# Kernel tuning notes

Hardware: AMD Instinct MI355X
Metric: run time of the kernel (lower is better)

Reference implementation:

```python
import jax, jax.numpy as jnp
import numpy as np

B, T, D = 512, 1024, 128
H = 256  # hidden_size
OUT = 1


def setup_inputs() -> dict:
    key = jax.random.key(0)
    ks = jax.random.split(key, 7)
    s1 = 1.0 / np.sqrt(D + H)
    s2 = 1.0 / np.sqrt(2 * H)
    so = 1.0 / np.sqrt(H)
    return {
        "x": jax.random.normal(ks[0], (B, T, D), dtype=jnp.float32),
        "W1": jax.random.normal(ks[1], (D + H, 4 * H), dtype=jnp.float32) * s1,
        "b1": jnp.zeros((4 * H,), dtype=jnp.float32),
        "W2": jax.random.normal(ks[2], (2 * H, 4 * H), dtype=jnp.float32) * s2,
        "b2": jnp.zeros((4 * H,), dtype=jnp.float32),
        "Wout": jax.random.normal(ks[3], (H, OUT), dtype=jnp.float32) * so,
        "bout": jnp.zeros((OUT,), dtype=jnp.float32),
    }


def _cell(h, c, inp, W, b, feats):
    # fused gates: Dense(4*features) on concat([inp, h]); order f, i, g, o
    gates = jnp.concatenate([inp, h], axis=-1) @ W + b
    f = jax.nn.sigmoid(gates[..., :feats])
    i = jax.nn.sigmoid(gates[..., feats:2 * feats])
    g = jnp.tanh(gates[..., 2 * feats:3 * feats])
    o = jax.nn.sigmoid(gates[..., 3 * feats:])
    new_c = f * c + i * g
    new_h = o * jnp.tanh(new_c)
    return new_h, new_c


def reference(x, W1, b1, W2, b2, Wout, bout):
    batch = x.shape[0]
    h1 = jnp.zeros((batch, H), dtype=x.dtype)
    c1 = jnp.zeros((batch, H), dtype=x.dtype)
    h2 = jnp.zeros((batch, H), dtype=x.dtype)
    c2 = jnp.zeros((batch, H), dtype=x.dtype)

    def step(carry, xt):
        h1, c1, h2, c2 = carry
        h1, c1 = _cell(h1, c1, xt, W1, b1, H)
        h2, c2 = _cell(h2, c2, h1, W2, b2, H)
        return (h1, c1, h2, c2), None

    xs = jnp.swapaxes(x, 0, 1)  # [T, B, D]
    (h1, c1, h2, c2), _ = jax.lax.scan(step, (h1, c1, h2, c2), xs)
    # dropout deterministic (training=False) -> identity; prediction from last h2
    return h2 @ Wout + bout
```

## Files before the change

### kernel.cpp

```cpp
#include <hip/hip_runtime.h>
#include <math.h>

#define Tlen  1024
#define Din   128
#define Hdim  256

typedef __attribute__((ext_vector_type(8)))  short short8;
typedef __attribute__((ext_vector_type(16))) short short16;
typedef __attribute__((ext_vector_type(4)))  float f32x4;

#define WS_BAR    0
#define WS_H      1024
#define WS_WLO1   2098176
#define WS_WLO2   2884608
#define ZERO_BYTES (1024 + 1048576)

__device__ __forceinline__ unsigned short f2bf(float f) {
    unsigned u = __float_as_uint(f);
    u += 0x7fffu + ((u >> 16) & 1u);
    return (unsigned short)(u >> 16);
}
__device__ __forceinline__ float bf2f(unsigned short s) {
    return __uint_as_float(((unsigned)s) << 16);
}
__device__ __forceinline__ float sigf(float x) { return 1.0f / (1.0f + __expf(-x)); }
__device__ __forceinline__ float tanh_(float x) {
    x = fminf(fmaxf(x, -15.0f), 15.0f);
    float e = __expf(2.0f * x);
    return (e - 1.0f) / (e + 1.0f);
}

__device__ __forceinline__ void afrag(const unsigned* p, short8& ah, short8& al) {
    union { unsigned long long u[4]; short16 v; } t;
    const unsigned long long* q = (const unsigned long long*)p;
    t.u[0] = __hip_atomic_load(q + 0, __ATOMIC_RELAXED, __HIP_MEMORY_SCOPE_AGENT);
    t.u[1] = __hip_atomic_load(q + 1, __ATOMIC_RELAXED, __HIP_MEMORY_SCOPE_AGENT);
    t.u[2] = __hip_atomic_load(q + 2, __ATOMIC_RELAXED, __HIP_MEMORY_SCOPE_AGENT);
    t.u[3] = __hip_atomic_load(q + 3, __ATOMIC_RELAXED, __HIP_MEMORY_SCOPE_AGENT);
    ah = __builtin_shufflevector(t.v, t.v, 0, 2, 4, 6, 8, 10, 12, 14);
    al = __builtin_shufflevector(t.v, t.v, 1, 3, 5, 7, 9, 11, 13, 15);
}

#define MFMA3(g, AH, AL, BH, BL)                                                   \
    acc[g] = __builtin_amdgcn_mfma_f32_16x16x32_bf16(AH, BH, acc[g], 0, 0, 0);     \
    acc[g] = __builtin_amdgcn_mfma_f32_16x16x32_bf16(AL, BH, acc[g], 0, 0, 0);     \
    acc[g] = __builtin_amdgcn_mfma_f32_16x16x32_bf16(AH, BL, acc[g], 0, 0, 0);

__global__ __launch_bounds__(256, 1) void lstm_persist(
    const float* __restrict__ x,
    const float* __restrict__ W1, const float* __restrict__ b1,
    const float* __restrict__ W2, const float* __restrict__ b2,
    const float* __restrict__ Wout, const float* __restrict__ bout,
    float* __restrict__ out, char* __restrict__ wsb)
{
    __shared__ short8 whi[4096];

    const int tid    = threadIdx.x;
    const int pod    = blockIdx.x & 7;
    const int member = blockIdx.x >> 3;
    const bool is_l1 = (member < 16);
    const int hs     = member & 15;
    const int NKS    = is_l1 ? 12 : 16;
    const float* Wraw = is_l1 ? W1 : W2;
    const float* bias = is_l1 ? b1 : b2;

    short8* blo = (short8*)(wsb + (is_l1 ? (WS_WLO1 + (size_t)hs * 49152)
                                         : (WS_WLO2 + (size_t)hs * 65536)));

    for (int t = tid; t < NKS * 256; t += 256) {
        const int lane = t & 63, g = (t >> 6) & 3, ks = t >> 8;
        const int q = lane >> 4, n = lane & 15;
        const int col = g * 256 + hs * 16 + n;
        short8 hv, lv;
#pragma unroll
        for (int j = 0; j < 8; ++j) {
            float v = Wraw[(size_t)(ks * 32 + q * 8 + j) * 1024 + col];
            unsigned short h = f2bf(v);
            hv[j] = (short)h;
            lv[j] = (short)f2bf(v - bf2f(h));
        }
        whi[t] = hv;
        blo[t] = lv;
    }
    __syncthreads();

    const int w = tid >> 6, lane = tid & 63;
    const int q = lane >> 4, n = lane & 15;
    const int rowA = pod * 64 + w * 16 + n;

    float biasg[4];
#pragma unroll
    for (int g = 0; g < 4; ++g) biasg[g] = bias[g * 256 + hs * 16 + n];

    float creg[4] = {0.f, 0.f, 0.f, 0.f};
    unsigned* bar = (unsigned*)(wsb + WS_BAR) + pod * 32;

    auto plane = [&](int par, int layer) -> unsigned* {
        return (unsigned*)(wsb + WS_H + (size_t)(par ^ 1) * 1048576 + (size_t)layer * 524288);
    };

    for (int p = 0; p <= Tlen; ++p) {
        f32x4 acc[4];
        const bool act_l1 = is_l1 && (p < Tlen);
        const bool act_l2 = (!is_l1) && (p >= 1);

        if (act_l1 || act_l2) {
#pragma unroll
            for (int g = 0; g < 4; ++g) {
                acc[g][0] = biasg[g]; acc[g][1] = biasg[g];
                acc[g][2] = biasg[g]; acc[g][3] = biasg[g];
            }
        }

        if (act_l1) {
#pragma unroll
            for (int ks = 0; ks < 4; ++ks) {
                const int kk = ks * 32 + q * 8;
                const float* xp = x + (size_t)rowA * (size_t)(Tlen * Din) + (size_t)p * Din + kk;
                f32x4 v0 = *(const f32x4*)xp;
                f32x4 v1 = *(const f32x4*)(xp + 4);
                float vv[8] = {v0[0], v0[1], v0[2], v0[3], v1[0], v1[1], v1[2], v1[3]};
                short8 ah, al;
#pragma unroll
                for (int j = 0; j < 8; ++j) {
                    unsigned short h = f2bf(vv[j]);
                    ah[j] = (short)h;
                    al[j] = (short)f2bf(vv[j] - bf2f(h));
                }
#pragma unroll
                for (int g = 0; g < 4; ++g) {
                    short8 bh = whi[ks * 256 + g * 64 + lane];
                    short8 bl = blo[ks * 256 + g * 64 + lane];
                    MFMA3(g, ah, al, bh, bl)
                }
            }
        }

        if (tid == 0 && p > 0) {
            const unsigned tgt = 32u * (unsigned)p;
            while (__hip_atomic_load(bar, __ATOMIC_RELAXED, __HIP_MEMORY_SCOPE_AGENT) < tgt) {}
        }
        __syncthreads();

        if (act_l1) {
            const int s = p;
            const unsigned* h1o = plane((s + 1) & 1, 0);
#pragma unroll
            for (int ks = 4; ks < 12; ++ks) {
                const int kk = ks * 32 + q * 8 - Din;
                short8 ah, al;
                afrag(h1o + (size_t)rowA * Hdim + kk, ah, al);
#pragma unroll
                for (int g = 0; g < 4; ++g) {
                    short8 bh = whi[ks * 256 + g * 64 + lane];
                    short8 bl = blo[ks * 256 + g * 64 + lane];
                    MFMA3(g, ah, al, bh, bl)
                }
            }
            unsigned* op = plane(s & 1, 0);
#pragma unroll
            for (int r = 0; r < 4; ++r) {
                float fg = acc[0][r], ig = acc[1][r], gg = acc[2][r], og = acc[3][r];
                float cn = sigf(fg) * creg[r] + sigf(ig) * tanh_(gg);
                creg[r] = cn;
                float hv = sigf(og) * tanh_(cn);
                const int row = pod * 64 + w * 16 + q * 4 + r;
                const int ci  = hs * 16 + n;
                unsigned short hh = f2bf(hv);
                unsigned short ll = f2bf(hv - bf2f(hh));
                unsigned word = (unsigned)hh | ((unsigned)ll << 16);
                __hip_atomic_store(op + (size_t)row * Hdim + ci, word,
                                   __ATOMIC_RELAXED, __HIP_MEMORY_SCOPE_AGENT);
            }
        }

        if (act_l2) {
            const int s = p - 1;
            const unsigned* h1c = plane(s & 1, 0);
            const unsigned* h2o = plane((s + 1) & 1, 1);
#pragma unroll
            for (int ks = 0; ks < 8; ++ks) {
                const int kk = ks * 32 + q * 8;
                short8 ah, al;
                afrag(h1c + (size_t)rowA * Hdim + kk, ah, al);
#pragma unroll
                for (int g = 0; g < 4; ++g) {
                    short8 bh = whi[ks * 256 + g * 64 + lane];
                    short8 bl = blo[ks * 256 + g * 64 + lane];
                    MFMA3(g, ah, al, bh, bl)
                }
            }
#pragma unroll
            for (int ks = 8; ks < 16; ++ks) {
                const int kk = ks * 32 + q * 8 - 256;
                short8 ah, al;
                afrag(h2o + (size_t)rowA * Hdim + kk, ah, al);
#pragma unroll
                for (int g = 0; g < 4; ++g) {
                    short8 bh = whi[ks * 256 + g * 64 + lane];
                    short8 bl = blo[ks * 256 + g * 64 + lane];
                    MFMA3(g, ah, al, bh, bl)
                }
            }
            unsigned* op = plane(s & 1, 1);
#pragma unroll
            for (int r = 0; r < 4; ++r) {
                float fg = acc[0][r], ig = acc[1][r], gg = acc[2][r], og = acc[3][r];
                float cn = sigf(fg) * creg[r] + sigf(ig) * tanh_(gg);
                creg[r] = cn;
                float hv = sigf(og) * tanh_(cn);
                const int row = pod * 64 + w * 16 + q * 4 + r;
                const int ci  = hs * 16 + n;
                unsigned short hh = f2bf(hv);
                unsigned short ll = f2bf(hv - bf2f(hh));
                unsigned word = (unsigned)hh | ((unsigned)ll << 16);
                __hip_atomic_store(op + (size_t)row * Hdim + ci, word,
                                   __ATOMIC_RELAXED, __HIP_MEMORY_SCOPE_AGENT);
            }
        }

        __syncthreads();
        if (tid == 0) {
            __hip_atomic_fetch_add(bar, 1u, __ATOMIC_RELAXED, __HIP_MEMORY_SCOPE_AGENT);
        }
    }

    if (member == 0) {
        if (tid == 0) {
            const unsigned tgt = 32u * (unsigned)(Tlen + 1);
            while (__hip_atomic_load(bar, __ATOMIC_RELAXED, __HIP_MEMORY_SCOPE_AGENT) < tgt) {}
        }
        __syncthreads();
        const unsigned* h2f = plane(1, 1);
        const int r = tid >> 2, part = tid & 3;
        const int row = pod * 64 + r;
        float s = 0.f;
        for (int k = part * 64; k < part * 64 + 64; k += 2) {
            unsigned long long u = __hip_atomic_load(
                (const unsigned long long*)(h2f + (size_t)row * Hdim + k),
                __ATOMIC_RELAXED, __HIP_MEMORY_SCOPE_AGENT);
            unsigned w0 = (unsigned)u, w1 = (unsigned)(u >> 32);
            float hv0 = bf2f((unsigned short)(w0 & 0xffff)) + bf2f((unsigned short)(w0 >> 16));
            float hv1 = bf2f((unsigned short)(w1 & 0xffff)) + bf2f((unsigned short)(w1 >> 16));
            s += hv0 * Wout[k] + hv1 * Wout[k + 1];
        }
        s += __shfl_xor(s, 1);
        s += __shfl_xor(s, 2);
        if (part == 0) out[row] = s + bout[0];
    }
}

extern "C" void kernel_launch(void* const* d_in, const int* in_sizes, int n_in,
                              void* d_out, int out_size, void* d_ws, size_t ws_size,
                              hipStream_t stream)
{
    const float* x    = (const float*)d_in[0];
    const float* W1   = (const float*)d_in[1];
    const float* b1   = (const float*)d_in[2];
    const float* W2   = (const float*)d_in[3];
    const float* b2   = (const float*)d_in[4];
    const float* Wout = (const float*)d_in[5];
    const float* bout = (const float*)d_in[6];

    hipMemsetAsync(d_ws, 0, ZERO_BYTES, stream);
    lstm_persist<<<256, 256, 0, stream>>>(x, W1, b1, W2, b2, Wout, bout,
                                          (float*)d_out, (char*)d_ws);
}
```

Baseline: 14.16 ms.

## Replace atomic counter barrier with per-member flags and batch h-state loads

Each block now publishes its progress by storing the step index into its own flag slot, and a whole wave polls all 32 pod flags in parallel with a vote and brief sleep, instead of every block doing fetch_add on one shared counter. This targets contention and serialization on a single atomic per timestep. The recurrent hidden-state fragments are also loaded into register buffers up front, before the MFMA loops, so loads overlap rather than alternating with compute. This raises register pressure and relies on relaxed ordering for the flag handoff.

```diff
diff --git a/kernel.cpp b/kernel.cpp
--- a/kernel.cpp
+++ b/kernel.cpp
@@ -30,21 +30,19 @@
     return (e - 1.0f) / (e + 1.0f);
 }
 
-__device__ __forceinline__ void afrag(const unsigned* p, short8& ah, short8& al) {
-    union { unsigned long long u[4]; short16 v; } t;
-    const unsigned long long* q = (const unsigned long long*)p;
-    t.u[0] = __hip_atomic_load(q + 0, __ATOMIC_RELAXED, __HIP_MEMORY_SCOPE_AGENT);
-    t.u[1] = __hip_atomic_load(q + 1, __ATOMIC_RELAXED, __HIP_MEMORY_SCOPE_AGENT);
-    t.u[2] = __hip_atomic_load(q + 2, __ATOMIC_RELAXED, __HIP_MEMORY_SCOPE_AGENT);
-    t.u[3] = __hip_atomic_load(q + 3, __ATOMIC_RELAXED, __HIP_MEMORY_SCOPE_AGENT);
-    ah = __builtin_shufflevector(t.v, t.v, 0, 2, 4, 6, 8, 10, 12, 14);
-    al = __builtin_shufflevector(t.v, t.v, 1, 3, 5, 7, 9, 11, 13, 15);
-}
-
 #define MFMA3(g, AH, AL, BH, BL)                                                   \
     acc[g] = __builtin_amdgcn_mfma_f32_16x16x32_bf16(AH, BH, acc[g], 0, 0, 0);     \
     acc[g] = __builtin_amdgcn_mfma_f32_16x16x32_bf16(AL, BH, acc[g], 0, 0, 0);     \
     acc[g] = __builtin_amdgcn_mfma_f32_16x16x32_bf16(AH, BL, acc[g], 0, 0, 0);
+
+#define UNPACK4(BUF, BASEI, AH, AL)                                                \
+    {                                                                              \
+        union { unsigned long long u[4]; short16 v; } t_;                          \
+        t_.u[0] = BUF[(BASEI) + 0]; t_.u[1] = BUF[(BASEI) + 1];                    \
+        t_.u[2] = BUF[(BASEI) + 2]; t_.u[3] = BUF[(BASEI) + 3];                    \
+        AH = __builtin_shufflevector(t_.v, t_.v, 0, 2, 4, 6, 8, 10, 12, 14);       \
+        AL = __builtin_shufflevector(t_.v, t_.v, 1, 3, 5, 7, 9, 11, 13, 15);       \
+    }
 
 __global__ __launch_bounds__(256, 1) void lstm_persist(
     const float* __restrict__ x,
@@ -93,7 +91,7 @@
     for (int g = 0; g < 4; ++g) biasg[g] = bias[g * 256 + hs * 16 + n];
 
     float creg[4] = {0.f, 0.f, 0.f, 0.f};
-    unsigned* bar = (unsigned*)(wsb + WS_BAR) + pod * 32;
+    unsigned* flags = (unsigned*)(wsb + WS_BAR) + pod * 32;
 
     auto plane = [&](int par, int layer) -> unsigned* {
         return (unsigned*)(wsb + WS_H + (size_t)(par ^ 1) * 1048576 + (size_t)layer * 524288);
@@ -136,20 +134,35 @@
             }
         }
 
-        if (tid == 0 && p > 0) {
-            const unsigned tgt = 32u * (unsigned)p;
-            while (__hip_atomic_load(bar, __ATOMIC_RELAXED, __HIP_MEMORY_SCOPE_AGENT) < tgt) {}
+        if (p > 0 && w == 0) {
+            const unsigned tgt = (unsigned)p;
+            const int fl = lane & 31;
+            for (;;) {
+                unsigned v = __hip_atomic_load(flags + fl, __ATOMIC_RELAXED,
+                                               __HIP_MEMORY_SCOPE_AGENT);
+                if (__all((int)(v >= tgt))) break;
+                __builtin_amdgcn_s_sleep(1);
+            }
         }
         __syncthreads();
 
         if (act_l1) {
             const int s = p;
             const unsigned* h1o = plane((s + 1) & 1, 0);
-#pragma unroll
-            for (int ks = 4; ks < 12; ++ks) {
-                const int kk = ks * 32 + q * 8 - Din;
+            const unsigned long long* hb =
+                (const unsigned long long*)(h1o + (size_t)rowA * Hdim);
+            unsigned long long buf[32];
+#pragma unroll
+            for (int i = 0; i < 32; ++i) {
+                const int ks0 = i >> 2, j = i & 3;
+                buf[i] = __hip_atomic_load(hb + ks0 * 16 + q * 4 + j,
+                                           __ATOMIC_RELAXED, __HIP_MEMORY_SCOPE_AGENT);
+            }
+#pragma unroll
+            for (int ks0 = 0; ks0 < 8; ++ks0) {
                 short8 ah, al;
-                afrag(h1o + (size_t)rowA * Hdim + kk, ah, al);
+                UNPACK4(buf, ks0 * 4, ah, al)
+                const int ks = ks0 + 4;
 #pragma unroll
                 for (int g = 0; g < 4; ++g) {
                     short8 bh = whi[ks * 256 + g * 64 + lane];
@@ -178,11 +191,27 @@
             const int s = p - 1;
             const unsigned* h1c = plane(s & 1, 0);
             const unsigned* h2o = plane((s + 1) & 1, 1);
+            const unsigned long long* hb1 =
+                (const unsigned long long*)(h1c + (size_t)rowA * Hdim);
+            const unsigned long long* hb2 =
+                (const unsigned long long*)(h2o + (size_t)rowA * Hdim);
+            unsigned long long bufA[32], bufB[32];
+#pragma unroll
+            for (int i = 0; i < 32; ++i) {
+                const int ks0 = i >> 2, j = i & 3;
+                bufA[i] = __hip_atomic_load(hb1 + ks0 * 16 + q * 4 + j,
+                                            __ATOMIC_RELAXED, __HIP_MEMORY_SCOPE_AGENT);
+            }
+#pragma unroll
+            for (int i = 0; i < 32; ++i) {
+                const int ks0 = i >> 2, j = i & 3;
+                bufB[i] = __hip_atomic_load(hb2 + ks0 * 16 + q * 4 + j,
+                                            __ATOMIC_RELAXED, __HIP_MEMORY_SCOPE_AGENT);
+            }
 #pragma unroll
             for (int ks = 0; ks < 8; ++ks) {
-                const int kk = ks * 32 + q * 8;
                 short8 ah, al;
-                afrag(h1c + (size_t)rowA * Hdim + kk, ah, al);
+                UNPACK4(bufA, ks * 4, ah, al)
 #pragma unroll
                 for (int g = 0; g < 4; ++g) {
                     short8 bh = whi[ks * 256 + g * 64 + lane];
@@ -191,10 +220,10 @@
                 }
             }
 #pragma unroll
-            for (int ks = 8; ks < 16; ++ks) {
-                const int kk = ks * 32 + q * 8 - 256;
+            for (int ks0 = 0; ks0 < 8; ++ks0) {
                 short8 ah, al;
-                afrag(h2o + (size_t)rowA * Hdim + kk, ah, al);
+                UNPACK4(bufB, ks0 * 4, ah, al)
+                const int ks = ks0 + 8;
 #pragma unroll
                 for (int g = 0; g < 4; ++g) {
                     short8 bh = whi[ks * 256 + g * 64 + lane];
@@ -221,14 +250,21 @@
 
         __syncthreads();
         if (tid == 0) {
-            __hip_atomic_fetch_add(bar, 1u, __ATOMIC_RELAXED, __HIP_MEMORY_SCOPE_AGENT);
+            __hip_atomic_store(flags + member, (unsigned)(p + 1),
+                               __ATOMIC_RELAXED, __HIP_MEMORY_SCOPE_AGENT);
         }
     }
 
     if (member == 0) {
-        if (tid == 0) {
-            const unsigned tgt = 32u * (unsigned)(Tlen + 1);
-            while (__hip_atomic_load(bar, __ATOMIC_RELAXED, __HIP_MEMORY_SCOPE_AGENT) < tgt) {}
+        if (w == 0) {
+            const unsigned tgt = (unsigned)(Tlen + 1);
+            const int fl = lane & 31;
+            for (;;) {
+                unsigned v = __hip_atomic_load(flags + fl, __ATOMIC_RELAXED,
+                                               __HIP_MEMORY_SCOPE_AGENT);
+                if (__all((int)(v >= tgt))) break;
+                __builtin_amdgcn_s_sleep(1);
+            }
         }
         __syncthreads();
         const unsigned* h2f = plane(1, 1);
```

Measured after the change: 16.81 ms. 1.19x slower.
